# Optimization experiments

Measured on AMD Instinct MI355X. Metric: run time of the kernel, lower is better.

Reference implementation:

```python
import jax, jax.numpy as jnp
import numpy as np

N = 50000        # nodes
E = 800000       # edges (avg degree 16)
F = 64           # in/out feature dim (scatter into zeros_like(x) forces out==in)
H = 128          # hidden dim
CIN = 2 * F + 1  # combined_features dim


def setup_inputs() -> dict:
    key = jax.random.key(0)
    ks = jax.random.split(key, 12)
    x = jax.random.normal(ks[0], (N, F), dtype=jnp.float32)
    pos = jax.random.normal(ks[1], (N, 3), dtype=jnp.float32)
    edge_index = jax.random.randint(ks[2], (2, E), 0, N, dtype=jnp.int64)
    s1 = 1.0 / np.sqrt(CIN)
    s2 = 1.0 / np.sqrt(H)
    W1x = jax.random.uniform(ks[3], (CIN, H), jnp.float32, -s1, s1)
    b1x = jax.random.uniform(ks[4], (H,), jnp.float32, -s1, s1)
    W2x = jax.random.uniform(ks[5], (H, F), jnp.float32, -s2, s2)
    b2x = jax.random.uniform(ks[6], (F,), jnp.float32, -s2, s2)
    W1p = jax.random.uniform(ks[7], (CIN, H), jnp.float32, -s1, s1)
    b1p = jax.random.uniform(ks[8], (H,), jnp.float32, -s1, s1)
    W2p = jax.random.uniform(ks[9], (H, 1), jnp.float32, -s2, s2)
    b2p = jax.random.uniform(ks[10], (1,), jnp.float32, -s2, s2)
    return {"x": x, "pos": pos, "edge_index": edge_index,
            "W1x": W1x, "b1x": b1x, "W2x": W2x, "b2x": b2x,
            "W1p": W1p, "b1p": b1p, "W2p": W2p, "b2p": b2p}


def reference(x, pos, edge_index, W1x, b1x, W2x, b2x, W1p, b1p, W2p, b2p):
    row, col = edge_index[0], edge_index[1]
    rel_pos = pos[row] - pos[col]                              # [E, 3]
    dist_sq = jnp.sum(rel_pos * rel_pos, axis=-1, keepdims=True)  # [E, 1]
    combined = jnp.concatenate([x[row], x[col], dist_sq], axis=-1)  # [E, 2F+1]
    # phi_x: Linear -> SiLU -> Linear
    msg_x = jax.nn.silu(combined @ W1x + b1x) @ W2x + b2x      # [E, F]
    aggregated_x = jax.ops.segment_sum(msg_x, col, num_segments=x.shape[0])
    # phi_pos: Linear -> SiLU -> Linear (scalar weight per edge)
    weight_pos = jax.nn.silu(combined @ W1p + b1p) @ W2p + b2p  # [E, 1]
    pos_update = weight_pos * rel_pos                           # [E, 3]
    aggregated_pos = jax.ops.segment_sum(pos_update, col, num_segments=pos.shape[0])
    return aggregated_x, aggregated_pos
```

## Files before the change

kernel.cpp:

```cpp
#include <hip/hip_runtime.h>

typedef short short8 __attribute__((ext_vector_type(8)));
typedef float floatx4 __attribute__((ext_vector_type(4)));

__device__ __forceinline__ unsigned short f2bf(float f) {
  unsigned int u = __float_as_uint(f);
  u += 0x7FFFu + ((u >> 16) & 1u);
  return (unsigned short)(u >> 16);
}

#if __has_builtin(__builtin_amdgcn_cvt_pk_bf16_f32)
typedef __bf16 bf16x2_t __attribute__((ext_vector_type(2)));
__device__ __forceinline__ unsigned int pk2bf(float lo, float hi) {
  bf16x2_t v = __builtin_amdgcn_cvt_pk_bf16_f32(lo, hi);
  return __builtin_bit_cast(unsigned int, v);
}
#else
__device__ __forceinline__ unsigned int pk2bf(float lo, float hi) {
  return (unsigned)f2bf(lo) | ((unsigned)f2bf(hi) << 16);
}
#endif

__global__ __launch_bounds__(256) void k_setup(
    float* __restrict__ out, int out_n,
    int* __restrict__ hist, int N,
    const float* __restrict__ x, unsigned short* __restrict__ xb, int nx,
    const float* __restrict__ W1x, const float* __restrict__ W1p,
    const float* __restrict__ W2x, unsigned short* __restrict__ wbuf,
    int b1, int b2, int b3)
{
  int blk = blockIdx.x, t = threadIdx.x;
  if (blk < b1) {
    int i = (blk * 256 + t) * 4;
    if (i + 4 <= out_n) {
      *(float4*)(out + i) = make_float4(0.f, 0.f, 0.f, 0.f);
    } else {
      for (int k = i; k < out_n; ++k) out[k] = 0.f;
    }
  } else if (blk < b2) {
    int i = (blk - b1) * 256 + t;
    if (i < N) hist[i] = 0;
  } else if (blk < b3) {
    int i = ((blk - b2) * 256 + t) * 8;
    if (i < nx) {
      float4 a = *(const float4*)(x + i);
      float4 b = *(const float4*)(x + i + 4);
      uint4 o;
      o.x = pk2bf(a.x, a.y); o.y = pk2bf(a.z, a.w);
      o.z = pk2bf(b.x, b.y); o.w = pk2bf(b.z, b.w);
      *(uint4*)(xb + i) = o;
    }
  } else {
    int i = (blk - b3) * 256 + t;
    if (i >= 40960) return;
    int jj = i & 7, lane = (i >> 3) & 63, ks = (i >> 9) & 3;
    int k = ks*32 + (lane >> 4)*8 + jj;
    float v;
    if (i < 32768) {
      const float* W = (i < 16384) ? W1x : W1p;
      int nt = (i >> 11) & 7;
      v = W[k*128 + nt*16 + (lane & 15)];
    } else {
      int nt = (i >> 11) & 3;
      v = W2x[k*64 + nt*16 + (lane & 15)];
    }
    wbuf[i] = f2bf(v);
  }
}

__global__ void k_hist(const int* __restrict__ col, int E, int* __restrict__ hist) {
  int i = blockIdx.x * 256 + threadIdx.x;
  if (i < E) atomicAdd(&hist[col[i]], 1);
}

__global__ __launch_bounds__(256) void k_scan_a(const int* __restrict__ hist, int N,
                                                int* __restrict__ excl, int* __restrict__ bsum) {
  __shared__ int wtot[4], wexc[4];
  int t = threadIdx.x, lane = t & 63, w = t >> 6;
  int base = blockIdx.x * 1024 + t * 4;
  int v0 = (base + 0 < N) ? hist[base + 0] : 0;
  int v1 = (base + 1 < N) ? hist[base + 1] : 0;
  int v2 = (base + 2 < N) ? hist[base + 2] : 0;
  int v3 = (base + 3 < N) ? hist[base + 3] : 0;
  int T = v0 + v1 + v2 + v3;
  int inc = T;
  #pragma unroll
  for (int s = 1; s < 64; s <<= 1) {
    int u = __shfl_up(inc, s, 64);
    if (lane >= s) inc += u;
  }
  if (lane == 63) wtot[w] = inc;
  __syncthreads();
  if (t == 0) {
    int a = 0;
    #pragma unroll
    for (int i = 0; i < 4; ++i) { wexc[i] = a; a += wtot[i]; }
    bsum[blockIdx.x] = a;
  }
  __syncthreads();
  int tex = wexc[w] + (inc - T);
  if (base + 0 < N) excl[base + 0] = tex;
  if (base + 1 < N) excl[base + 1] = tex + v0;
  if (base + 2 < N) excl[base + 2] = tex + v0 + v1;
  if (base + 3 < N) excl[base + 3] = tex + v0 + v1 + v2;
}

__global__ __launch_bounds__(256) void k_scatter(
    const int* __restrict__ row, const int* __restrict__ col, int E,
    int* __restrict__ excl, const int* __restrict__ bsum, int NB,
    int2* __restrict__ sedge) {
  __shared__ int boff_sh[64];
  int t = threadIdx.x;
  if (t < 64) {
    int v = (t < NB) ? bsum[t] : 0;
    int inc = v;
    #pragma unroll
    for (int s = 1; s < 64; s <<= 1) {
      int u = __shfl_up(inc, s, 64);
      if (t >= s) inc += u;
    }
    boff_sh[t] = inc - v;
  }
  __syncthreads();
  int i = blockIdx.x * 256 + t;
  if (i < E) {
    int c = col[i];
    int p = atomicAdd(&excl[c], 1) + boff_sh[c >> 10];
    sedge[p] = make_int2(row[i], c);
  }
}

__global__ __launch_bounds__(512) void mp_main(
    const float* __restrict__ x, const unsigned short* __restrict__ xb, int use_xb,
    const float* __restrict__ pos,
    const int2* __restrict__ sedge,
    const int* __restrict__ rowp, const int* __restrict__ colp,
    int E, int sorted,
    const float* __restrict__ W1x, const float* __restrict__ b1x,
    const float* __restrict__ W1p, const float* __restrict__ b1p,
    const float* __restrict__ b2x, const float* __restrict__ W2p,
    const float* __restrict__ b2p,
    const unsigned short* __restrict__ wbuf,
    float* __restrict__ out_x, float* __restrict__ out_pos)
{
  __shared__ __align__(16) unsigned short C_lds[64][136];
  __shared__ __align__(16) unsigned short H_lds[64][136];
  __shared__ float dsq_sh[64];
  __shared__ float rel_lds[64][3];
  __shared__ int   col_sh[64];
  __shared__ float wsum[8][64];

  const int t    = threadIdx.x;
  const int e0   = blockIdx.x * 64;
  const int wv   = t >> 6;
  const int lane = t & 63;
  const int quad = lane >> 4;
  const int lc   = lane & 15;

  if (t < 64) {
    int e = e0 + t;
    float rp0 = 0.f, rp1 = 0.f, rp2 = 0.f, dsq = 0.f; int c = -1;
    if (e < E) {
      int r;
      if (sorted) { int2 rc = sedge[e]; r = rc.x; c = rc.y; }
      else        { r = rowp[e]; c = colp[e]; }
      float pr0 = pos[r*3+0], pr1 = pos[r*3+1], pr2 = pos[r*3+2];
      float pc0 = pos[c*3+0], pc1 = pos[c*3+1], pc2 = pos[c*3+2];
      rp0 = pr0 - pc0; rp1 = pr1 - pc1; rp2 = pr2 - pc2;
      dsq = rp0*rp0 + rp1*rp1 + rp2*rp2;
    }
    rel_lds[t][0] = rp0; rel_lds[t][1] = rp1; rel_lds[t][2] = rp2;
    col_sh[t] = c;
    dsq_sh[t] = dsq;
  }
  {
    const int s = t >> 3, p = t & 7;
    const int e = e0 + s;
    uint4 rv, cv;
    if (e < E) {
      int r, c;
      if (sorted) { int2 rc = sedge[e]; r = rc.x; c = rc.y; }
      else        { r = rowp[e]; c = colp[e]; }
      if (use_xb) {
        rv = *(const uint4*)(xb + (size_t)r*64 + p*8);
        cv = *(const uint4*)(xb + (size_t)c*64 + p*8);
      } else {
        const float4* xr = (const float4*)(x + (size_t)r*64 + p*8);
        const float4* xc = (const float4*)(x + (size_t)c*64 + p*8);
        float4 a0 = xr[0], a1 = xr[1];
        float4 d0 = xc[0], d1 = xc[1];
        rv = make_uint4(pk2bf(a0.x,a0.y), pk2bf(a0.z,a0.w), pk2bf(a1.x,a1.y), pk2bf(a1.z,a1.w));
        cv = make_uint4(pk2bf(d0.x,d0.y), pk2bf(d0.z,d0.w), pk2bf(d1.x,d1.y), pk2bf(d1.z,d1.w));
      }
    } else {
      rv = cv = make_uint4(0u, 0u, 0u, 0u);
    }
    *(uint4*)&C_lds[s][p*8]      = rv;
    *(uint4*)&C_lds[s][64 + p*8] = cv;
  }

  const short8* __restrict__ w1x_f = (const short8*)(wbuf);
  const short8* __restrict__ w1p_f = (const short8*)(wbuf + 16384);
  const short8* __restrict__ w2x_f = (const short8*)(wbuf + 32768);

  const int ht = wv;
  const int ft = wv & 3;
  short8 a1x[4], a1p[4], a2w[4];
  #pragma unroll
  for (int ks = 0; ks < 4; ++ks) {
    a1x[ks] = w1x_f[(ht*4 + ks)*64 + lane];
    a1p[ks] = w1p_f[(ht*4 + ks)*64 + lane];
    a2w[ks] = w2x_f[(ft*4 + ks)*64 + lane];
  }
  const int hidx = ht*16 + quad*4;
  const int fidx = ft*16 + quad*4;
  float w128x[4], b1xv[4], w128p[4], b1pv[4], wp2v[4], b2xr[4];
  #pragma unroll
  for (int r = 0; r < 4; ++r) {
    w128x[r] = W1x[16384 + hidx + r];
    b1xv[r]  = b1x[hidx + r];
    w128p[r] = W1p[16384 + hidx + r];
    b1pv[r]  = b1p[hidx + r];
    wp2v[r]  = W2p[hidx + r];
    b2xr[r]  = b2x[fidx + r];
  }
  const float b2ps = b2p[0];
  __syncthreads();

  #pragma unroll 1
  for (int et = 0; et < 4; ++et) {
    floatx4 ax = {0,0,0,0}, ap = {0,0,0,0};
    #pragma unroll
    for (int ks = 0; ks < 4; ++ks) {
      short8 b = *(const short8*)&C_lds[et*16 + lc][ks*32 + quad*8];
      ax = __builtin_amdgcn_mfma_f32_16x16x32_bf16(a1x[ks], b, ax, 0, 0, 0);
      ap = __builtin_amdgcn_mfma_f32_16x16x32_bf16(a1p[ks], b, ap, 0, 0, 0);
    }
    const float dsqv = dsq_sh[et*16 + lc];
    float ps = 0.f, sx[4];
    #pragma unroll
    for (int r = 0; r < 4; ++r) {
      float hx = ax[r] + dsqv*w128x[r] + b1xv[r];
      sx[r] = hx * __builtin_amdgcn_rcpf(1.f + __expf(-hx));
      float hp = ap[r] + dsqv*w128p[r] + b1pv[r];
      float sp = hp * __builtin_amdgcn_rcpf(1.f + __expf(-hp));
      ps += sp * wp2v[r];
    }
    *(uint2*)&H_lds[et*16 + lc][ht*16 + quad*4] =
        make_uint2(pk2bf(sx[0], sx[1]), pk2bf(sx[2], sx[3]));
    ps += __shfl_xor(ps, 16, 64);
    ps += __shfl_xor(ps, 32, 64);
    if (lane < 16) wsum[wv][et*16 + lane] = ps;
  }
  __syncthreads();

  const int etb = (wv >> 2) * 2;
  #pragma unroll
  for (int eti = 0; eti < 2; ++eti) {
    const int et = etb + eti;
    floatx4 acc = {0,0,0,0};
    #pragma unroll
    for (int ks = 0; ks < 4; ++ks) {
      short8 b = *(const short8*)&H_lds[et*16 + lc][ks*32 + quad*8];
      acc = __builtin_amdgcn_mfma_f32_16x16x32_bf16(a2w[ks], b, acc, 0, 0, 0);
    }
    int edge = et*16 + lc;
    int myc = col_sh[edge];
    float v0 = acc[0] + b2xr[0], v1 = acc[1] + b2xr[1];
    float v2 = acc[2] + b2xr[2], v3 = acc[3] + b2xr[3];
    if (sorted) {
      #pragma unroll
      for (int s = 1; s < 16; s <<= 1) {
        int   nc  = __shfl_down(myc, s, 64);
        float n0  = __shfl_down(v0,  s, 64);
        float n1  = __shfl_down(v1,  s, 64);
        float n2  = __shfl_down(v2,  s, 64);
        float n3  = __shfl_down(v3,  s, 64);
        if ((lc + s < 16) && (nc == myc)) { v0 += n0; v1 += n1; v2 += n2; v3 += n3; }
      }
    }
    bool head = (myc >= 0) && (!sorted || lc == 0 || col_sh[edge-1] != myc);
    if (head) {
      float* dst = out_x + (size_t)myc*64 + ft*16 + quad*4;
      atomicAdd(dst + 0, v0);
      atomicAdd(dst + 1, v1);
      atomicAdd(dst + 2, v2);
      atomicAdd(dst + 3, v3);
    }
  }

  if (t < 64) {
    int c = col_sh[t];
    float w = wsum[0][t] + wsum[1][t] + wsum[2][t] + wsum[3][t]
            + wsum[4][t] + wsum[5][t] + wsum[6][t] + wsum[7][t] + b2ps;
    float p0 = w * rel_lds[t][0], p1 = w * rel_lds[t][1], p2 = w * rel_lds[t][2];
    if (sorted) {
      #pragma unroll
      for (int s = 1; s < 64; s <<= 1) {
        int   nc = __shfl_down(c,  s, 64);
        float n0 = __shfl_down(p0, s, 64);
        float n1 = __shfl_down(p1, s, 64);
        float n2 = __shfl_down(p2, s, 64);
        if ((t + s < 64) && (nc == c)) { p0 += n0; p1 += n1; p2 += n2; }
      }
    }
    bool head = (c >= 0) && (!sorted || t == 0 || col_sh[t-1] != c);
    if (head) {
      atomicAdd(&out_pos[(size_t)c*3 + 0], p0);
      atomicAdd(&out_pos[(size_t)c*3 + 1], p1);
      atomicAdd(&out_pos[(size_t)c*3 + 2], p2);
    }
  }
}

extern "C" void kernel_launch(void* const* d_in, const int* in_sizes, int n_in,
                              void* d_out, int out_size, void* d_ws, size_t ws_size,
                              hipStream_t stream) {
  const float* x   = (const float*)d_in[0];
  const float* pos = (const float*)d_in[1];
  const int*   ei  = (const int*)d_in[2];
  const float* W1x = (const float*)d_in[3];
  const float* b1x = (const float*)d_in[4];
  const float* W2x = (const float*)d_in[5];
  const float* b2x = (const float*)d_in[6];
  const float* W1p = (const float*)d_in[7];
  const float* b1p = (const float*)d_in[8];
  const float* W2p = (const float*)d_in[9];
  const float* b2p = (const float*)d_in[10];

  const int E = in_sizes[2] / 2;
  const int N = in_sizes[0] / 64;
  const int* rowp = ei;
  const int* colp = ei + E;
  float* out_x   = (float*)d_out;
  float* out_pos = out_x + (size_t)N * 64;

  char* ws = (char*)d_ws;
  const size_t xb_bytes = (size_t)N * 64 * 2;
  size_t base = 0;
  int use_xb = 0;
  {
    size_t needA = xb_bytes + 81920 + 200192 + 512 + (size_t)E * 8;
    if (ws_size >= needA) { use_xb = 1; base = xb_bytes; }
  }
  unsigned short* xb   = (unsigned short*)ws;
  unsigned short* wbuf = (unsigned short*)(ws + base);
  int*  off   = (int*)(ws + base + 81920);
  int*  bsum  = (int*)(ws + base + 81920 + 200192);
  int2* sedge = (int2*)(ws + base + 81920 + 200192 + 512);
  const size_t need_sort = base + 81920 + 200192 + 512 + (size_t)E * 8;
  const int use_sort = (ws_size >= need_sort) ? 1 : 0;

  const int nx = N * 64;
  const int nb_out  = (out_size + 1023) / 1024;
  const int nb_hist = use_sort ? (N + 255) / 256 : 0;
  const int nb_xcvt = use_xb ? (nx + 2047) / 2048 : 0;
  const int nb_prep = 160;
  const int b1 = nb_out, b2 = b1 + nb_hist, b3 = b2 + nb_xcvt;
  const int setup_blocks = b3 + nb_prep;
  k_setup<<<setup_blocks, 256, 0, stream>>>(
      (float*)d_out, out_size, off, N, x, xb, nx,
      W1x, W1p, W2x, wbuf, b1, b2, b3);

  if (use_sort) {
    const int NB = (N + 1023) / 1024;
    k_hist<<<(E + 255) / 256, 256, 0, stream>>>(colp, E, off);
    k_scan_a<<<NB, 256, 0, stream>>>(off, N, off, bsum);
    k_scatter<<<(E + 255) / 256, 256, 0, stream>>>(rowp, colp, E, off, bsum, NB, sedge);
  }

  mp_main<<<(E + 63) / 64, 512, 0, stream>>>(x, xb, use_xb, pos, sedge, rowp, colp,
                                             E, use_sort,
                                             W1x, b1x, W1p, b1p, b2x, W2p, b2p,
                                             wbuf, out_x, out_pos);
}
```

Before: 359.8 us.

## Precompute per-node first-layer projections and gather them per edge

The first linear layer is split algebraically: x[row]@W1_top and x[col]@W1_mid are computed once per node by a new MFMA kernel and stored as packed bf16 tables for both the x and pos branches. The edge kernel then only gathers two 512-byte rows per edge, adds them with the dist_sq term, and applies SiLU, removing the per-edge first-layer matmul. The histogram is folded into the setup kernel with vectorized atomics, and the counts are zeroed with a memset. The cost is extra workspace and a gather of twice as many bytes per edge. Intermediates are now rounded to bf16 before the add, which adds some error.

```diff
diff --git a/kernel.cpp b/kernel.cpp
--- a/kernel.cpp
+++ b/kernel.cpp
@@ -21,13 +21,16 @@
 }
 #endif
 
+__device__ __forceinline__ float silu(float h) {
+  return h * __builtin_amdgcn_rcpf(1.f + __expf(-h));
+}
+
 __global__ __launch_bounds__(256) void k_setup(
     float* __restrict__ out, int out_n,
-    int* __restrict__ hist, int N,
-    const float* __restrict__ x, unsigned short* __restrict__ xb, int nx,
+    const int* __restrict__ colp, int E, int* __restrict__ hist,
     const float* __restrict__ W1x, const float* __restrict__ W1p,
     const float* __restrict__ W2x, unsigned short* __restrict__ wbuf,
-    int b1, int b2, int b3)
+    int b1, int b2)
 {
   int blk = blockIdx.x, t = threadIdx.x;
   if (blk < b1) {
@@ -38,20 +41,16 @@
       for (int k = i; k < out_n; ++k) out[k] = 0.f;
     }
   } else if (blk < b2) {
-    int i = (blk - b1) * 256 + t;
-    if (i < N) hist[i] = 0;
-  } else if (blk < b3) {
-    int i = ((blk - b2) * 256 + t) * 8;
-    if (i < nx) {
-      float4 a = *(const float4*)(x + i);
-      float4 b = *(const float4*)(x + i + 4);
-      uint4 o;
-      o.x = pk2bf(a.x, a.y); o.y = pk2bf(a.z, a.w);
-      o.z = pk2bf(b.x, b.y); o.w = pk2bf(b.z, b.w);
-      *(uint4*)(xb + i) = o;
+    int i = ((blk - b1) * 256 + t) * 4;
+    if (i + 4 <= E) {
+      int4 c = *(const int4*)(colp + i);
+      atomicAdd(&hist[c.x], 1); atomicAdd(&hist[c.y], 1);
+      atomicAdd(&hist[c.z], 1); atomicAdd(&hist[c.w], 1);
+    } else {
+      for (int k = i; k < E; ++k) atomicAdd(&hist[colp[k]], 1);
     }
   } else {
-    int i = (blk - b3) * 256 + t;
+    int i = (blk - b2) * 256 + t;
     if (i >= 40960) return;
     int jj = i & 7, lane = (i >> 3) & 63, ks = (i >> 9) & 3;
     int k = ks*32 + (lane >> 4)*8 + jj;
@@ -68,9 +67,81 @@
   }
 }
 
-__global__ void k_hist(const int* __restrict__ col, int E, int* __restrict__ hist) {
-  int i = blockIdx.x * 256 + threadIdx.x;
-  if (i < E) atomicAdd(&hist[col[i]], 1);
+__global__ __launch_bounds__(256) void k_nodeA(
+    const float* __restrict__ x, const unsigned short* __restrict__ wbuf,
+    const float* __restrict__ b1x, const float* __restrict__ b1p, int N,
+    unsigned int* __restrict__ Ar, unsigned int* __restrict__ Ac)
+{
+  __shared__ __align__(16) unsigned short xt[64][72];
+  const int t = threadIdx.x, n0 = blockIdx.x * 64;
+  const int wv = t >> 6, lane = t & 63, quad = lane >> 4, lc = lane & 15;
+
+  {
+    int nd = t >> 2, p = t & 3;
+    int n = n0 + nd;
+    uint4 o0, o1;
+    if (n < N) {
+      const float4* xp = (const float4*)(x + (size_t)n*64 + p*16);
+      float4 a = xp[0], b = xp[1], c = xp[2], d = xp[3];
+      o0 = make_uint4(pk2bf(a.x,a.y), pk2bf(a.z,a.w), pk2bf(b.x,b.y), pk2bf(b.z,b.w));
+      o1 = make_uint4(pk2bf(c.x,c.y), pk2bf(c.z,c.w), pk2bf(d.x,d.y), pk2bf(d.z,d.w));
+    } else {
+      o0 = o1 = make_uint4(0u,0u,0u,0u);
+    }
+    *(uint4*)&xt[nd][p*16]     = o0;
+    *(uint4*)&xt[nd][p*16 + 8] = o1;
+  }
+
+  const short8* __restrict__ w1x_f = (const short8*)wbuf;
+  const short8* __restrict__ w1p_f = (const short8*)(wbuf + 16384);
+  short8 fxr[2][2], fxc[2][2], fpr[2][2], fpc[2][2];
+  float bx[2], bp[2];
+  #pragma unroll
+  for (int ti = 0; ti < 2; ++ti) {
+    int nt = wv + 4*ti;
+    #pragma unroll
+    for (int k2 = 0; k2 < 2; ++k2) {
+      fxr[ti][k2] = w1x_f[(nt*4 + k2)*64 + lane];
+      fxc[ti][k2] = w1x_f[(nt*4 + 2 + k2)*64 + lane];
+      fpr[ti][k2] = w1p_f[(nt*4 + k2)*64 + lane];
+      fpc[ti][k2] = w1p_f[(nt*4 + 2 + k2)*64 + lane];
+    }
+    bx[ti] = b1x[nt*16 + lc];
+    bp[ti] = b1p[nt*16 + lc];
+  }
+  __syncthreads();
+
+  #pragma unroll 1
+  for (int mw = 0; mw < 4; ++mw) {
+    short8 a0 = *(const short8*)&xt[mw*16 + lc][quad*8];
+    short8 a1 = *(const short8*)&xt[mw*16 + lc][32 + quad*8];
+    floatx4 xr[2], xc[2], pr[2], pc[2];
+    #pragma unroll
+    for (int ti = 0; ti < 2; ++ti) {
+      xr[ti] = (floatx4){0,0,0,0}; xc[ti] = (floatx4){0,0,0,0};
+      pr[ti] = (floatx4){0,0,0,0}; pc[ti] = (floatx4){0,0,0,0};
+      xr[ti] = __builtin_amdgcn_mfma_f32_16x16x32_bf16(a0, fxr[ti][0], xr[ti], 0,0,0);
+      xr[ti] = __builtin_amdgcn_mfma_f32_16x16x32_bf16(a1, fxr[ti][1], xr[ti], 0,0,0);
+      xc[ti] = __builtin_amdgcn_mfma_f32_16x16x32_bf16(a0, fxc[ti][0], xc[ti], 0,0,0);
+      xc[ti] = __builtin_amdgcn_mfma_f32_16x16x32_bf16(a1, fxc[ti][1], xc[ti], 0,0,0);
+      pr[ti] = __builtin_amdgcn_mfma_f32_16x16x32_bf16(a0, fpr[ti][0], pr[ti], 0,0,0);
+      pr[ti] = __builtin_amdgcn_mfma_f32_16x16x32_bf16(a1, fpr[ti][1], pr[ti], 0,0,0);
+      pc[ti] = __builtin_amdgcn_mfma_f32_16x16x32_bf16(a0, fpc[ti][0], pc[ti], 0,0,0);
+      pc[ti] = __builtin_amdgcn_mfma_f32_16x16x32_bf16(a1, fpc[ti][1], pc[ti], 0,0,0);
+    }
+    #pragma unroll
+    for (int ti = 0; ti < 2; ++ti) {
+      int h = (wv + 4*ti)*16 + lc;
+      #pragma unroll
+      for (int rr = 0; rr < 4; ++rr) {
+        int nd = n0 + mw*16 + quad*4 + rr;
+        if (nd < N) {
+          Ar[(size_t)nd*128 + h] = pk2bf(xr[ti][rr] + bx[ti], pr[ti][rr] + bp[ti]);
+          Ac[(size_t)nd*128 + h] = pk2bf(xc[ti][rr], pc[ti][rr]);
+        }
+      }
+    }
+  }
 }
 
 __global__ __launch_bounds__(256) void k_scan_a(const int* __restrict__ hist, int N,
@@ -130,9 +201,158 @@
   }
 }
 
-__global__ __launch_bounds__(512) void mp_main(
-    const float* __restrict__ x, const unsigned short* __restrict__ xb, int use_xb,
+__global__ __launch_bounds__(256) void mp_main(
     const float* __restrict__ pos,
+    const int2* __restrict__ sedge,
+    const int* __restrict__ rowp, const int* __restrict__ colp,
+    int E, int sorted,
+    const unsigned int* __restrict__ Ar, const unsigned int* __restrict__ Ac,
+    const float* __restrict__ W1x, const float* __restrict__ W1p,
+    const float* __restrict__ b2x, const float* __restrict__ W2p,
+    const float* __restrict__ b2p,
+    const unsigned short* __restrict__ wbuf,
+    float* __restrict__ out_x, float* __restrict__ out_pos)
+{
+  __shared__ __align__(16) unsigned short H_lds[64][136];
+  __shared__ __align__(16) uint4 edata[64];
+  __shared__ float rel_lds[64][3];
+  __shared__ int   col_sh[64];
+  __shared__ float wsum[4][64];
+
+  const int t    = threadIdx.x;
+  const int e0   = blockIdx.x * 64;
+  const int wv   = t >> 6;
+  const int lane = t & 63;
+  const int quad = lane >> 4;
+  const int lc   = lane & 15;
+
+  if (t < 64) {
+    int e = e0 + t;
+    int r = 0, c = 0, cs = -1;
+    float rp0 = 0.f, rp1 = 0.f, rp2 = 0.f, dsq = 0.f;
+    if (e < E) {
+      if (sorted) { int2 rc = sedge[e]; r = rc.x; c = rc.y; }
+      else        { r = rowp[e]; c = colp[e]; }
+      cs = c;
+      float pr0 = pos[r*3+0], pr1 = pos[r*3+1], pr2 = pos[r*3+2];
+      float pc0 = pos[c*3+0], pc1 = pos[c*3+1], pc2 = pos[c*3+2];
+      rp0 = pr0 - pc0; rp1 = pr1 - pc1; rp2 = pr2 - pc2;
+      dsq = rp0*rp0 + rp1*rp1 + rp2*rp2;
+    }
+    rel_lds[t][0] = rp0; rel_lds[t][1] = rp1; rel_lds[t][2] = rp2;
+    col_sh[t] = cs;
+    edata[t] = make_uint4((unsigned)r, (unsigned)c, __float_as_uint(dsq), 0u);
+  }
+
+  const short8* __restrict__ w2x_f = (const short8*)(wbuf + 32768);
+  short8 a2w[4];
+  #pragma unroll
+  for (int ks = 0; ks < 4; ++ks) a2w[ks] = w2x_f[(wv*4 + ks)*64 + lane];
+
+  float w1xd[2][4], w1pd[2][4], wp2[2][4], b2xr[4];
+  #pragma unroll
+  for (int ti = 0; ti < 2; ++ti)
+    #pragma unroll
+    for (int r = 0; r < 4; ++r) {
+      int h = (wv + 4*ti)*16 + quad*4 + r;
+      w1xd[ti][r] = W1x[16384 + h];
+      w1pd[ti][r] = W1p[16384 + h];
+      wp2[ti][r]  = W2p[h];
+    }
+  #pragma unroll
+  for (int r = 0; r < 4; ++r) b2xr[r] = b2x[wv*16 + quad*4 + r];
+  const float b2ps = b2p[0];
+  __syncthreads();
+
+  #pragma unroll 2
+  for (int et = 0; et < 4; ++et) {
+    uint4 ed = edata[et*16 + lc];
+    const float dsqv = __uint_as_float(ed.z);
+    float ps = 0.f;
+    #pragma unroll
+    for (int ti = 0; ti < 2; ++ti) {
+      const int ht = wv + 4*ti;
+      const int hb = ht*32 + quad*8;
+      uint4 va = *(const uint4*)((const unsigned short*)Ar + (size_t)ed.x*256 + hb);
+      uint4 vc = *(const uint4*)((const unsigned short*)Ac + (size_t)ed.y*256 + hb);
+      float sx[4];
+      #pragma unroll
+      for (int j = 0; j < 4; ++j) {
+        unsigned a = (&va.x)[j], b = (&vc.x)[j];
+        float hx = __uint_as_float(a << 16) + __uint_as_float(b << 16)
+                 + dsqv * w1xd[ti][j];
+        float hp = __uint_as_float(a & 0xffff0000u) + __uint_as_float(b & 0xffff0000u)
+                 + dsqv * w1pd[ti][j];
+        sx[j] = silu(hx);
+        ps += silu(hp) * wp2[ti][j];
+      }
+      *(uint2*)&H_lds[et*16 + lc][ht*16 + quad*4] =
+          make_uint2(pk2bf(sx[0], sx[1]), pk2bf(sx[2], sx[3]));
+    }
+    ps += __shfl_xor(ps, 16, 64);
+    ps += __shfl_xor(ps, 32, 64);
+    if (lane < 16) wsum[wv][et*16 + lane] = ps;
+  }
+  __syncthreads();
+
+  #pragma unroll 2
+  for (int et = 0; et < 4; ++et) {
+    floatx4 acc = {0,0,0,0};
+    #pragma unroll
+    for (int ks = 0; ks < 4; ++ks) {
+      short8 b = *(const short8*)&H_lds[et*16 + lc][ks*32 + quad*8];
+      acc = __builtin_amdgcn_mfma_f32_16x16x32_bf16(a2w[ks], b, acc, 0, 0, 0);
+    }
+    int edge = et*16 + lc;
+    int myc = col_sh[edge];
+    float v0 = acc[0] + b2xr[0], v1 = acc[1] + b2xr[1];
+    float v2 = acc[2] + b2xr[2], v3 = acc[3] + b2xr[3];
+    if (sorted) {
+      #pragma unroll
+      for (int s = 1; s < 16; s <<= 1) {
+        int   nc = __shfl_down(myc, s, 64);
+        float n0 = __shfl_down(v0,  s, 64);
+        float n1 = __shfl_down(v1,  s, 64);
+        float n2 = __shfl_down(v2,  s, 64);
+        float n3 = __shfl_down(v3,  s, 64);
+        if ((lc + s < 16) && (nc == myc)) { v0 += n0; v1 += n1; v2 += n2; v3 += n3; }
+      }
+    }
+    bool head = (myc >= 0) && (!sorted || lc == 0 || col_sh[edge-1] != myc);
+    if (head) {
+      float* dst = out_x + (size_t)myc*64 + wv*16 + quad*4;
+      atomicAdd(dst + 0, v0);
+      atomicAdd(dst + 1, v1);
+      atomicAdd(dst + 2, v2);
+      atomicAdd(dst + 3, v3);
+    }
+  }
+
+  if (t < 64) {
+    int c = col_sh[t];
+    float w = wsum[0][t] + wsum[1][t] + wsum[2][t] + wsum[3][t] + b2ps;
+    float p0 = w * rel_lds[t][0], p1 = w * rel_lds[t][1], p2 = w * rel_lds[t][2];
+    if (sorted) {
+      #pragma unroll
+      for (int s = 1; s < 64; s <<= 1) {
+        int   nc = __shfl_down(c,  s, 64);
+        float n0 = __shfl_down(p0, s, 64);
+        float n1 = __shfl_down(p1, s, 64);
+        float n2 = __shfl_down(p2, s, 64);
+        if ((t + s < 64) && (nc == c)) { p0 += n0; p1 += n1; p2 += n2; }
+      }
+    }
+    bool head = (c >= 0) && (!sorted || t == 0 || col_sh[t-1] != c);
+    if (head) {
+      atomicAdd(&out_pos[(size_t)c*3 + 0], p0);
+      atomicAdd(&out_pos[(size_t)c*3 + 1], p1);
+      atomicAdd(&out_pos[(size_t)c*3 + 2], p2);
+    }
+  }
+}
+
+__global__ __launch_bounds__(512) void mp_legacy(
+    const float* __restrict__ x, const float* __restrict__ pos,
     const int2* __restrict__ sedge,
     const int* __restrict__ rowp, const int* __restrict__ colp,
     int E, int sorted,
@@ -181,17 +401,12 @@
       int r, c;
       if (sorted) { int2 rc = sedge[e]; r = rc.x; c = rc.y; }
       else        { r = rowp[e]; c = colp[e]; }
-      if (use_xb) {
-        rv = *(const uint4*)(xb + (size_t)r*64 + p*8);
-        cv = *(const uint4*)(xb + (size_t)c*64 + p*8);
-      } else {
-        const float4* xr = (const float4*)(x + (size_t)r*64 + p*8);
-        const float4* xc = (const float4*)(x + (size_t)c*64 + p*8);
-        float4 a0 = xr[0], a1 = xr[1];
-        float4 d0 = xc[0], d1 = xc[1];
-        rv = make_uint4(pk2bf(a0.x,a0.y), pk2bf(a0.z,a0.w), pk2bf(a1.x,a1.y), pk2bf(a1.z,a1.w));
-        cv = make_uint4(pk2bf(d0.x,d0.y), pk2bf(d0.z,d0.w), pk2bf(d1.x,d1.y), pk2bf(d1.z,d1.w));
-      }
+      const float4* xr = (const float4*)(x + (size_t)r*64 + p*8);
+      const float4* xc = (const float4*)(x + (size_t)c*64 + p*8);
+      float4 a0 = xr[0], a1 = xr[1];
+      float4 d0 = xc[0], d1 = xc[1];
+      rv = make_uint4(pk2bf(a0.x,a0.y), pk2bf(a0.z,a0.w), pk2bf(a1.x,a1.y), pk2bf(a1.z,a1.w));
+      cv = make_uint4(pk2bf(d0.x,d0.y), pk2bf(d0.z,d0.w), pk2bf(d1.x,d1.y), pk2bf(d1.z,d1.w));
     } else {
       rv = cv = make_uint4(0u, 0u, 0u, 0u);
     }
@@ -241,10 +456,9 @@
     #pragma unroll
     for (int r = 0; r < 4; ++r) {
       float hx = ax[r] + dsqv*w128x[r] + b1xv[r];
-      sx[r] = hx * __builtin_amdgcn_rcpf(1.f + __expf(-hx));
+      sx[r] = silu(hx);
       float hp = ap[r] + dsqv*w128p[r] + b1pv[r];
-      float sp = hp * __builtin_amdgcn_rcpf(1.f + __expf(-hp));
-      ps += sp * wp2v[r];
+      ps += silu(hp) * wp2v[r];
     }
     *(uint2*)&H_lds[et*16 + lc][ht*16 + quad*4] =
         make_uint2(pk2bf(sx[0], sx[1]), pk2bf(sx[2], sx[3]));
@@ -271,11 +485,11 @@
     if (sorted) {
       #pragma unroll
       for (int s = 1; s < 16; s <<= 1) {
-        int   nc  = __shfl_down(myc, s, 64);
-        float n0  = __shfl_down(v0,  s, 64);
-        float n1  = __shfl_down(v1,  s, 64);
-        float n2  = __shfl_down(v2,  s, 64);
-        float n3  = __shfl_down(v3,  s, 64);
+        int   nc = __shfl_down(myc, s, 64);
+        float n0 = __shfl_down(v0,  s, 64);
+        float n1 = __shfl_down(v1,  s, 64);
+        float n2 = __shfl_down(v2,  s, 64);
+        float n3 = __shfl_down(v3,  s, 64);
         if ((lc + s < 16) && (nc == myc)) { v0 += n0; v1 += n1; v2 += n2; v3 += n3; }
       }
     }
@@ -335,42 +549,47 @@
   float* out_x   = (float*)d_out;
   float* out_pos = out_x + (size_t)N * 64;
 
+  const size_t tab_one  = (size_t)N * 512;
+  const size_t tab_sz   = 2 * tab_one;
+  const size_t rest_sz  = 81920 + 200192 + 512 + (size_t)E * 8;
+  const int use_tab  = (ws_size >= tab_sz + rest_sz) ? 1 : 0;
+  const size_t base  = use_tab ? tab_sz : 0;
+  const int use_sort = (ws_size >= base + rest_sz) ? 1 : 0;
+
   char* ws = (char*)d_ws;
-  const size_t xb_bytes = (size_t)N * 64 * 2;
-  size_t base = 0;
-  int use_xb = 0;
-  {
-    size_t needA = xb_bytes + 81920 + 200192 + 512 + (size_t)E * 8;
-    if (ws_size >= needA) { use_xb = 1; base = xb_bytes; }
-  }
-  unsigned short* xb   = (unsigned short*)ws;
+  unsigned int*   Ar   = (unsigned int*)ws;
+  unsigned int*   Ac   = (unsigned int*)(ws + tab_one);
   unsigned short* wbuf = (unsigned short*)(ws + base);
   int*  off   = (int*)(ws + base + 81920);
   int*  bsum  = (int*)(ws + base + 81920 + 200192);
   int2* sedge = (int2*)(ws + base + 81920 + 200192 + 512);
-  const size_t need_sort = base + 81920 + 200192 + 512 + (size_t)E * 8;
-  const int use_sort = (ws_size >= need_sort) ? 1 : 0;
-
-  const int nx = N * 64;
+
+  if (use_sort) hipMemsetAsync(off, 0, (size_t)N * sizeof(int), stream);
+
   const int nb_out  = (out_size + 1023) / 1024;
-  const int nb_hist = use_sort ? (N + 255) / 256 : 0;
-  const int nb_xcvt = use_xb ? (nx + 2047) / 2048 : 0;
+  const int nb_hist = use_sort ? (E/4 + 255) / 256 + 1 : 0;
   const int nb_prep = 160;
-  const int b1 = nb_out, b2 = b1 + nb_hist, b3 = b2 + nb_xcvt;
-  const int setup_blocks = b3 + nb_prep;
-  k_setup<<<setup_blocks, 256, 0, stream>>>(
-      (float*)d_out, out_size, off, N, x, xb, nx,
-      W1x, W1p, W2x, wbuf, b1, b2, b3);
+  const int b1 = nb_out, b2 = b1 + nb_hist;
+  k_setup<<<b2 + nb_prep, 256, 0, stream>>>(
+      (float*)d_out, out_size, colp, use_sort ? E : 0, off,
+      W1x, W1p, W2x, wbuf, b1, b2);
+
+  if (use_tab)
+    k_nodeA<<<(N + 63) / 64, 256, 0, stream>>>(x, wbuf, b1x, b1p, N, Ar, Ac);
 
   if (use_sort) {
     const int NB = (N + 1023) / 1024;
-    k_hist<<<(E + 255) / 256, 256, 0, stream>>>(colp, E, off);
     k_scan_a<<<NB, 256, 0, stream>>>(off, N, off, bsum);
     k_scatter<<<(E + 255) / 256, 256, 0, stream>>>(rowp, colp, E, off, bsum, NB, sedge);
   }
 
-  mp_main<<<(E + 63) / 64, 512, 0, stream>>>(x, xb, use_xb, pos, sedge, rowp, colp,
-                                             E, use_sort,
-                                             W1x, b1x, W1p, b1p, b2x, W2p, b2p,
-                                             wbuf, out_x, out_pos);
-}
+  if (use_tab) {
+    mp_main<<<(E + 63) / 64, 256, 0, stream>>>(
+        pos, sedge, rowp, colp, E, use_sort,
+        Ar, Ac, W1x, W1p, b2x, W2p, b2p, wbuf, out_x, out_pos);
+  } else {
+    mp_legacy<<<(E + 63) / 64, 512, 0, stream>>>(
+        x, pos, sedge, rowp, colp, E, use_sort,
+        W1x, b1x, W1p, b1p, b2x, W2p, b2p, wbuf, out_x, out_pos);
+  }
+}
```

Measured after the change: 318.6 us. 11.5% less time.
